# Kernel optimization log

Hardware: AMD Instinct MI355X
Metric: run time of the kernel (lower is better)

The kernel has to match this reference:

```python
import jax, jax.numpy as jnp
import numpy as np
from jax import lax

BZ, CAP, SEQ, INV = 32, 134, 144, 16
E_SP, E_FT = 1072, 64


def sage(x, e_src, e_dst, Wl, bl, Wr, n_nodes):
    # PyG SAGEConv (mean aggr): out = lin_l(mean_{j->i} x_j) + lin_r(x_i)
    # x: [B, N, F]; edges broadcast over batch
    msgs = x[:, e_src]                                   # [B, E, F] gather
    agg = jnp.zeros_like(x).at[:, e_dst].add(msgs)        # [B, N, F] scatter-add
    deg = jnp.zeros((n_nodes,), x.dtype).at[e_dst].add(1.0)
    mean = agg / jnp.clip(deg, 1.0)[None, :, None]
    return mean @ Wl + bl + x @ Wr


def setup_inputs() -> dict:
    key = jax.random.key(0)
    ks = jax.random.split(key, 16)
    s = lambda fan: 1.0 / np.sqrt(fan)
    inp = {
        'src': jax.random.normal(ks[0], (BZ, CAP, SEQ, INV), jnp.float32),
        'graph_edge_index': jax.random.randint(ks[1], (2, E_SP), 0, CAP, jnp.int32),
        'feature_edge_index': jax.random.randint(ks[2], (2, E_FT), 0, INV, jnp.int32),
        # spatial SAGEConv(in_var, in_var)
        'gcn_Wl': jax.random.uniform(ks[3], (INV, INV), jnp.float32, -s(INV), s(INV)),
        'gcn_bl': jnp.zeros((INV,), jnp.float32),
        'gcn_Wr': jax.random.uniform(ks[4], (INV, INV), jnp.float32, -s(INV), s(INV)),
        # feature SAGEConv(seq_len, seq_len)
        'fgcn_Wl': jax.random.uniform(ks[5], (SEQ, SEQ), jnp.float32, -s(SEQ), s(SEQ)),
        'fgcn_bl': jnp.zeros((SEQ,), jnp.float32),
        'fgcn_Wr': jax.random.uniform(ks[6], (SEQ, SEQ), jnp.float32, -s(SEQ), s(SEQ)),
        # Conv1d(in_var, in_var, k=3/5, no bias): OIW layout
        'conv1_w': jax.random.uniform(ks[7], (INV, INV, 3), jnp.float32, -s(INV * 3), s(INV * 3)),
        'conv2_w': jax.random.uniform(ks[8], (INV, INV, 5), jnp.float32, -s(INV * 5), s(INV * 5)),
        # Linear(3*in_var, in_var)
        'fc_w': jax.random.uniform(ks[9], (3 * INV, INV), jnp.float32, -s(3 * INV), s(3 * INV)),
        'fc_b': jnp.zeros((INV,), jnp.float32),
    }
    return inp


def reference(src, graph_edge_index, feature_edge_index, gcn_Wl, gcn_bl, gcn_Wr,
              fgcn_Wl, fgcn_bl, fgcn_Wr, conv1_w, conv2_w, fc_w, fc_b):
    bz, cap, seq, inv = src.shape
    # --- spatial GCN: nodes = turbines, features = in_var, batched over bz*seq
    x1 = src.transpose(0, 2, 1, 3).reshape(bz * seq, cap, inv)
    sp = sage(x1, graph_edge_index[0], graph_edge_index[1], gcn_Wl, gcn_bl, gcn_Wr, cap)
    spatial_fea = sp.reshape(bz, seq, cap, inv).transpose(0, 2, 1, 3)
    # --- feature GCN: nodes = variables, features = seq_len, batched over bz*cap
    x2 = src.transpose(0, 1, 3, 2).reshape(bz * cap, inv, seq)
    ft = sage(x2, feature_edge_index[0], feature_edge_index[1], fgcn_Wl, fgcn_bl, fgcn_Wr, inv)
    fea_fea = ft.reshape(bz, cap, inv, seq).transpose(0, 1, 3, 2)
    # --- temporal dual Conv1d over seq axis, channels = in_var
    x3 = src.reshape(bz * cap, seq, inv).transpose(0, 2, 1)  # [N, C, L]
    dn = ('NCH', 'OIH', 'NCH')
    c1 = lax.conv_general_dilated(x3, conv1_w, (1,), [(1, 1)], dimension_numbers=dn)
    c2 = lax.conv_general_dilated(x3, conv2_w, (1,), [(2, 2)], dimension_numbers=dn)
    temporal_fea = (c1 + c2).transpose(0, 2, 1).reshape(bz, cap, seq, inv)
    # --- concat + FC fusion + residual (dropout = identity at eval)
    com = jnp.concatenate([spatial_fea, fea_fea, temporal_fea], axis=-1)  # [..., 3*inv]
    out = com @ fc_w + fc_b
    return src + out
```

## Files before the change

kernel.cpp:

```cpp
#include <hip/hip_runtime.h>
#include <hip/hip_bf16.h>

#define BZn 32
#define CAPn 134
#define SEQn 144
#define INVn 16
#define ESP 1072
#define EFT 64


typedef __attribute__((ext_vector_type(8))) short bf16x8;
typedef __attribute__((ext_vector_type(4))) short short4v;
typedef __attribute__((ext_vector_type(4))) float f32x4;

#define MFMA(a, b, c) __builtin_amdgcn_mfma_f32_16x16x32_bf16(a, b, c, 0, 0, 0)

__device__ __forceinline__ unsigned short f2bf(float f) {
    union { float f; unsigned u; } v; v.f = f;
    unsigned r = v.u + 0x7fff + ((v.u >> 16) & 1);
    return (unsigned short)(r >> 16);
}
__device__ __forceinline__ unsigned pk2(float a, float b) {
    float2 v; v.x = a; v.y = b;
    union { __hip_bfloat162 h; unsigned u; } c;
    c.h = __float22bfloat162_rn(v);
    return c.u;
}
__device__ __forceinline__ short4v pack4(f32x4 v) {
    union { unsigned u[2]; short4v s; } r;
    r.u[0] = pk2(v[0], v[1]);
    r.u[1] = pk2(v[2], v[3]);
    return r.s;
}

__global__ __launch_bounds__(256) void prep_kernel(
    const int* __restrict__ ge, const int* __restrict__ fe,
    const float* __restrict__ Wl,  const float* __restrict__ Wr,
    const float* __restrict__ fWl, const float* __restrict__ fWr,
    const float* __restrict__ w1,  const float* __restrict__ w2,
    const float* __restrict__ fcw, const float* __restrict__ bl,
    const float* __restrict__ fcb,
    int* __restrict__ ws)
{
    int t = threadIdx.x;
    char* wsb = (char*)ws;
    unsigned short* uB     = (unsigned short*)(wsb + 5376);
    unsigned short* vB     = (unsigned short*)(wsb + 6400);
    unsigned short* spB2   = (unsigned short*)(wsb + 7424);
    float*          biasf  = (float*)(wsb + 8448);
    unsigned short* convA2 = (unsigned short*)(wsb + 8704);
    unsigned short* featB  = (unsigned short*)(wsb + 12800);

    if (blockIdx.x == 0) {
        int* g_rp  = ws;
        int* g_col = ws + 135;
        float* g_inv = (float*)(ws + 1207);
        __shared__ int cnt[CAPn], off[CAPn];
        for (int c0 = t; c0 < CAPn; c0 += 256) cnt[c0] = 0;
        __syncthreads();
        for (int e = t; e < ESP; e += 256) atomicAdd(&cnt[ge[ESP + e]], 1);
        __syncthreads();
        if (t == 0) {
            int run = 0;
            for (int c0 = 0; c0 < CAPn; c0++) {
                off[c0] = run; g_rp[c0] = run;
                g_inv[c0] = 1.0f / fmaxf((float)cnt[c0], 1.0f);
                run += cnt[c0];
            }
            g_rp[CAPn] = run;
        }
        __syncthreads();
        for (int c0 = t; c0 < CAPn; c0 += 256) cnt[c0] = 0;
        __syncthreads();
        for (int e = t; e < ESP; e += 256) {
            int d = ge[ESP + e];
            int p = off[d] + atomicAdd(&cnt[d], 1);
            g_col[p] = ge[e];
        }
    } else if (blockIdx.x == 1) {
        __shared__ float sw[1312];
        __shared__ int fm[256];
        __shared__ float finv[16];
        for (int u = t; u < 768; u += 256) sw[u] = fcw[u];
        if (t < 256) sw[768 + t]  = Wl[t];
        if (t < 256) sw[1024 + t] = Wr[t];
        if (t < 16)  sw[1280 + t] = bl[t];
        if (t < 16)  sw[1296 + t] = fcb[t];
        fm[t] = 0;
        __syncthreads();
        if (t < EFT) atomicAdd(&fm[fe[t] * 16 + fe[EFT + t]], 1);
        __syncthreads();
        if (t < 16) {
            int dg = 0;
            for (int j = 0; j < 16; j++) dg += fm[j * 16 + t];
            finv[t] = 1.0f / fmaxf((float)dg, 1.0f);
        }
        __syncthreads();
        for (int u = t; u < 512; u += 256) {
            int l = u >> 3, j = u & 7, k = (l >> 4) * 8 + j, ip = l & 15;
            float vu = 0.f, vv = 0.f, vs = 0.f;
            if (k < 16) {
                for (int i = 0; i < 16; i++)
                    vu += (float)fm[k * 16 + i] * finv[i] * sw[(16 + i) * 16 + ip];
                vv = sw[(16 + k) * 16 + ip];
                for (int i = 0; i < 16; i++) vs += sw[768 + k * 16 + i] * sw[i * 16 + ip];
            } else {
                for (int i = 0; i < 16; i++) vs += sw[1024 + (k - 16) * 16 + i] * sw[i * 16 + ip];
            }
            uB[u] = f2bf(vu); vB[u] = f2bf(vv); spB2[u] = f2bf(vs);
        }
        if (t < 16) {
            float b0 = sw[1296 + t], c0 = 0.f;
            for (int i = 0; i < 16; i++) {
                b0 += sw[1280 + i] * sw[i * 16 + t];
                c0 += sw[(16 + i) * 16 + t];
            }
            biasf[t] = b0; biasf[16 + t] = c0;
        }
    } else if (blockIdx.x == 2) {
        __shared__ float swt[2816];
        for (int u = t; u < 768;  u += 256) swt[u]        = fcw[u];
        for (int u = t; u < 768;  u += 256) swt[768 + u]  = w1[u];
        for (int u = t; u < 1280; u += 256) swt[1536 + u] = w2[u];
        __syncthreads();
        for (int u = t; u < 2048; u += 256) {
            int kk2 = u >> 9, l = (u >> 3) & 63, j = u & 7, q = l >> 4, o = l & 15;
            int kkp = kk2 * 2 + (q >> 1), i = (q & 1) * 8 + j;
            float v = 0.f;
            for (int o0 = 0; o0 < 16; o0++) {
                float w = (kkp < 3) ? swt[768 + (o0 * 16 + i) * 3 + kkp]
                                    : swt[1536 + (o0 * 16 + i) * 5 + (kkp - 3)];
                v += w * swt[(32 + o0) * 16 + o];
            }
            convA2[u] = f2bf(v);
        }
    } else {
        __shared__ float wtile[32][145];
        int kk = blockIdx.x - 3;
        for (int u = t; u < 32 * 144; u += 256) {
            int r = u / 144, s = u - r * 144;
            int k = kk * 32 + r;
            wtile[r][s] = (k < 144) ? fWl[k * 144 + s] : fWr[(k - 144) * 144 + s];
        }
        __syncthreads();
        for (int u = t; u < 4608; u += 256) {
            int n0 = u >> 9, rem = u & 511;
            int l = rem >> 3, j = rem & 7;
            featB[(kk * 9 + n0) * 512 + rem] =
                f2bf(wtile[(l >> 4) * 8 + j][n0 * 16 + (l & 15)]);
        }
    }
}

__global__ __launch_bounds__(256, 4) void fused_kernel(
    const float* __restrict__ src,
    const float* __restrict__ fbl,
    const int* __restrict__ ws,
    float* __restrict__ out)
{
    const int* g_rp  = ws;
    const int* g_col = ws + 135;
    const float* g_inv = (const float*)(ws + 1207);
    const char* wsb = (const char*)ws;
    const unsigned short* uB     = (const unsigned short*)(wsb + 5376);
    const unsigned short* vB     = (const unsigned short*)(wsb + 6400);
    const unsigned short* spB2   = (const unsigned short*)(wsb + 7424);
    const float*          biasf  = (const float*)(wsb + 8448);
    const unsigned short* convA2 = (const unsigned short*)(wsb + 8704);
    const unsigned short* featB  = (const unsigned short*)(wsb + 12800);

    __shared__ __align__(16) char smem[24704];
    unsigned short* xs = (unsigned short*)smem;
    unsigned short* mt = (unsigned short*)(smem + 7104);
    unsigned short* uv = (unsigned short*)(smem + 14016);
    float* accF   = (float*)smem;
    float* s_fbl  = (float*)(smem + 24000);
    float* s_bias = (float*)(smem + 24576);
    float* s_cs   = (float*)(smem + 24640);

    int t = threadIdx.x;
    int wave = t >> 6, lane = t & 63;
    int q = lane >> 4, ln = lane & 15;

    int ust_w = (wave == 0) ? 0 : (2 * wave + 1);
    int sst_w = 2 * wave;

    int xcd  = blockIdx.x & 7;
    int slot = blockIdx.x >> 3;
    int bl_  = slot / 134;
    int c    = slot - bl_ * 134;
    int b    = xcd * 4 + bl_;
    int bc   = b * CAPn + c;
    const float* srcb = src + (size_t)b * (CAPn * SEQn * INVn);
    const float* srcc = srcb + (size_t)c * (SEQn * INVn);

    const f32x4* s4 = (const f32x4*)srcc;
    f32x4 x0 = s4[t], x1 = s4[t + 256];
    f32x4 x2 = {0.f,0.f,0.f,0.f};
    if (t < 64) x2 = s4[t + 512];

    int rs = g_rp[c], re = g_rp[c + 1];
    float idg = g_inv[c];
    f32x4 m0a = {0.f,0.f,0.f,0.f}, m1a = {0.f,0.f,0.f,0.f}, m2a = {0.f,0.f,0.f,0.f};
    f32x4 m0b = {0.f,0.f,0.f,0.f}, m1b = {0.f,0.f,0.f,0.f}, m2b = {0.f,0.f,0.f,0.f};
    int e = rs;
    for (; e + 3 < re; e += 4) {
        int n0_ = g_col[e], n1_ = g_col[e + 1], n2_ = g_col[e + 2], n3_ = g_col[e + 3];
        const f32x4* p0 = (const f32x4*)(srcb + (size_t)n0_ * (SEQn * INVn));
        const f32x4* p1 = (const f32x4*)(srcb + (size_t)n1_ * (SEQn * INVn));
        const f32x4* p2 = (const f32x4*)(srcb + (size_t)n2_ * (SEQn * INVn));
        const f32x4* p3 = (const f32x4*)(srcb + (size_t)n3_ * (SEQn * INVn));
        f32x4 a0 = p0[t],       a1 = p1[t],       a2 = p2[t],       a3 = p3[t];
        f32x4 b0 = p0[t + 256], b1 = p1[t + 256], b2 = p2[t + 256], b3 = p3[t + 256];
        f32x4 c0 = {0.f,0.f,0.f,0.f}, c1 = c0, c2 = c0, c3 = c0;
        if (t < 64) { c0 = p0[t + 512]; c1 = p1[t + 512]; c2 = p2[t + 512]; c3 = p3[t + 512]; }
        m0a += a0; m0b += a1; m1a += b0; m1b += b1;
        m0a += a2; m0b += a3; m1a += b2; m1b += b3;
        if (t < 64) { m2a += c0; m2b += c1; m2a += c2; m2b += c3; }
    }
    for (; e + 1 < re; e += 2) {
        int na = g_col[e], nb = g_col[e + 1];
        const f32x4* pa = (const f32x4*)(srcb + (size_t)na * (SEQn * INVn));
        const f32x4* pb = (const f32x4*)(srcb + (size_t)nb * (SEQn * INVn));
        m0a += pa[t];       m0b += pb[t];
        m1a += pa[t + 256]; m1b += pb[t + 256];
        if (t < 64) { m2a += pa[t + 512]; m2b += pb[t + 512]; }
    }
    if (e < re) {
        int na = g_col[e];
        const f32x4* pa = (const f32x4*)(srcb + (size_t)na * (SEQn * INVn));
        m0a += pa[t]; m1a += pa[t + 256];
        if (t < 64) m2a += pa[t + 512];
    }

    bf16x8 caf0 = *(const bf16x8*)(convA2 + (0 * 64 + lane) * 8);
    bf16x8 caf1 = *(const bf16x8*)(convA2 + (1 * 64 + lane) * 8);
    bf16x8 caf2 = *(const bf16x8*)(convA2 + (2 * 64 + lane) * 8);
    bf16x8 caf3 = *(const bf16x8*)(convA2 + (3 * 64 + lane) * 8);
    bf16x8 sbf = *(const bf16x8*)(spB2 + lane * 8);
    bf16x8 ubf = *(const bf16x8*)(uB + lane * 8);
    bf16x8 vbf = *(const bf16x8*)(vB + lane * 8);

    int s0g = t >> 2, i0g = (t & 3) * 4;
    f32x4 m0 = (m0a + m0b) * idg, m1 = (m1a + m1b) * idg, m2 = (m2a + m2b) * idg;
    *(short4v*)&mt[s0g * 24 + i0g]         = pack4(m0);
    *(short4v*)&mt[(64 + s0g) * 24 + i0g]  = pack4(m1);
    if (t < 64) *(short4v*)&mt[(128 + s0g) * 24 + i0g] = pack4(m2);

    *(short4v*)&xs[(s0g + 2) * 24 + i0g]        = pack4(x0);
    *(short4v*)&xs[(64 + s0g + 2) * 24 + i0g]   = pack4(x1);
    if (t < 64) *(short4v*)&xs[(128 + s0g + 2) * 24 + i0g] = pack4(x2);
    if (t < 64) {
        int r = t >> 4, i = t & 15;
        int row = (r < 2) ? r : 144 + r;
        xs[row * 24 + i] = 0;
    }
    if (t < SEQn) s_fbl[t] = fbl[t];
    if (t < 16) { s_bias[t] = biasf[t]; s_cs[t] = biasf[16 + t]; }
    __syncthreads();

    #pragma unroll
    for (int tt = 0; tt < 3; tt++) {
        if ((wave == 0) || (tt < 2)) {
            int mtt = ust_w + tt;
            int sl = mtt * 16 + ln;
            bf16x8 a = {0,0,0,0,0,0,0,0};
            if (q < 2) a = *(const bf16x8*)&xs[(sl + 2) * 24 + q * 8];
            f32x4 au = {0.f,0.f,0.f,0.f}, av = {0.f,0.f,0.f,0.f};
            au = MFMA(a, ubf, au);
            av = MFMA(a, vbf, av);
            *(short4v*)&uv[ln * 312 + mtt * 16 + q * 4]       = pack4(au);
            *(short4v*)&uv[ln * 312 + 144 + mtt * 16 + q * 4] = pack4(av);
        }
    }
    f32x4 accS0 = {0.f,0.f,0.f,0.f}, accS1 = accS0, accS2 = accS0;
    {
        int sl = (sst_w + 0) * 16 + ln;
        const unsigned short* ap = (q < 2) ? &mt[sl * 24 + (q & 1) * 8]
                                           : &xs[(sl + 2) * 24 + (q & 1) * 8];
        accS0 = MFMA(*(const bf16x8*)ap, sbf, accS0);
    }
    {
        int sl = (sst_w + 1) * 16 + ln;
        const unsigned short* ap = (q < 2) ? &mt[sl * 24 + (q & 1) * 8]
                                           : &xs[(sl + 2) * 24 + (q & 1) * 8];
        accS1 = MFMA(*(const bf16x8*)ap, sbf, accS1);
    }
    if (wave == 3) {
        int sl = (sst_w + 2) * 16 + ln;
        const unsigned short* ap = (q < 2) ? &mt[sl * 24 + (q & 1) * 8]
                                           : &xs[(sl + 2) * 24 + (q & 1) * 8];
        accS2 = MFMA(*(const bf16x8*)ap, sbf, accS2);
    }
    __syncthreads();

#define B_TILE(N0, ACC) { \
    int n0_t = (N0); int sl_t = n0_t * 16 + ln; \
    bf16x8 bfrag[9]; \
    _Pragma("unroll") \
    for (int kk = 0; kk < 9; kk++) \
        bfrag[kk] = *(const bf16x8*)(featB + ((kk * 9 + n0_t) * 64 + lane) * 8); \
    bf16x8 cb[4]; \
    _Pragma("unroll") \
    for (int kk = 0; kk < 4; kk++) { \
        int kkp = kk * 2 + (q >> 1); \
        int off = (kkp < 3) ? (kkp - 1) : (kkp - 5); \
        cb[kk] = *(const bf16x8*)&xs[(sl_t + 2 + off) * 24 + (q & 1) * 8]; } \
    f32x4 acc_ = {0.f,0.f,0.f,0.f}; \
    acc_ = MFMA(caf0, cb[0], acc_); \
    acc_ = MFMA(caf1, cb[1], acc_); \
    acc_ = MFMA(caf2, cb[2], acc_); \
    acc_ = MFMA(caf3, cb[3], acc_); \
    _Pragma("unroll") \
    for (int kk = 0; kk < 9; kk++) { \
        bf16x8 a_ = *(const bf16x8*)&uv[ln * 312 + kk * 32 + q * 8]; \
        acc_ = MFMA(a_, bfrag[kk], acc_); } \
    ACC = acc_; }

    f32x4 accB0 = {0.f,0.f,0.f,0.f}, accB1 = accB0, accB2 = accB0;
    B_TILE(ust_w + 0, accB0)
    B_TILE(ust_w + 1, accB1)
    if (wave == 0) B_TILE(ust_w + 2, accB2)
#undef B_TILE
    __syncthreads();

    *(f32x4*)&accF[(((ust_w + 0) * 16 + ln) * 16) + q * 4] = accB0;
    *(f32x4*)&accF[(((ust_w + 1) * 16 + ln) * 16) + q * 4] = accB1;
    if (wave == 0)
        *(f32x4*)&accF[(((ust_w + 2) * 16 + ln) * 16) + q * 4] = accB2;
    __syncthreads();

    #pragma unroll
    for (int r = 0; r < 4; r++)
        accF[((sst_w + 0) * 16 + q * 4 + r) * 16 + ln] += accS0[r];
    #pragma unroll
    for (int r = 0; r < 4; r++)
        accF[((sst_w + 1) * 16 + q * 4 + r) * 16 + ln] += accS1[r];
    if (wave == 3) {
        #pragma unroll
        for (int r = 0; r < 4; r++)
            accF[((sst_w + 2) * 16 + q * 4 + r) * 16 + ln] += accS2[r];
    }
    __syncthreads();

    f32x4* out4 = (f32x4*)(out + (size_t)bc * (SEQn * INVn));
    int i0 = (t & 3) * 4;
    f32x4 bias4 = *(const f32x4*)&s_bias[i0];
    f32x4 cs4   = *(const f32x4*)&s_cs[i0];
    {
        f32x4 a = *(const f32x4*)&accF[4 * t];
        out4[t] = a + x0 + bias4 + s_fbl[t >> 2] * cs4;
    }
    {
        f32x4 a = *(const f32x4*)&accF[4 * (t + 256)];
        out4[t + 256] = a + x1 + bias4 + s_fbl[(t + 256) >> 2] * cs4;
    }
    if (t < 64) {
        f32x4 a = *(const f32x4*)&accF[4 * (t + 512)];
        out4[t + 512] = a + x2 + bias4 + s_fbl[(t + 512) >> 2] * cs4;
    }
}

extern "C" void kernel_launch(void* const* d_in, const int* in_sizes, int n_in,
                              void* d_out, int out_size, void* d_ws, size_t ws_size,
                              hipStream_t stream)
{
    const float* src = (const float*)d_in[0];
    const int* ge = (const int*)d_in[1];
    const int* fe = (const int*)d_in[2];
    const float* Wl  = (const float*)d_in[3];
    const float* blp = (const float*)d_in[4];
    const float* Wr  = (const float*)d_in[5];
    const float* fWl = (const float*)d_in[6];
    const float* fbl = (const float*)d_in[7];
    const float* fWr = (const float*)d_in[8];
    const float* w1  = (const float*)d_in[9];
    const float* w2  = (const float*)d_in[10];
    const float* fcw = (const float*)d_in[11];
    const float* fcb = (const float*)d_in[12];
    float* out = (float*)d_out;
    int* ws = (int*)d_ws;

    hipLaunchKernelGGL(prep_kernel, dim3(12), dim3(256), 0, stream,
                       ge, fe, Wl, Wr, fWl, fWr, w1, w2, fcw, blp, fcb, ws);
    hipLaunchKernelGGL(fused_kernel, dim3(BZn * CAPn), dim3(256), 0, stream,
                       src, fbl, ws, out);
}
```

Before: 150.8 us.

## Replace mean-tile LDS staging with cross-lane bpermute and pad accumulator rows

The neighbour-mean tile is no longer written to shared memory and read back for the spatial MFMA. Each wave now pulls its operands straight from registers with ds_bpermute, reassigning tiles so every wave handles the rows it already holds. This cuts LDS footprint, which may allow more resident blocks, and removes one store/load round trip. The fp32 accumulator buffer also gets a 20-float row stride instead of 16 to reduce bank conflicts in the transposed adds, at the cost of bpermute instructions and more index arithmetic.

After: 150.7 us. Within noise of the previous version (-0.0%).

```diff
diff --git a/kernel.cpp b/kernel.cpp
--- a/kernel.cpp
+++ b/kernel.cpp
@@ -169,21 +169,19 @@
     const unsigned short* convA2 = (const unsigned short*)(wsb + 8704);
     const unsigned short* featB  = (const unsigned short*)(wsb + 12800);
 
-    __shared__ __align__(16) char smem[24704];
+    __shared__ __align__(16) char smem[17792];
     unsigned short* xs = (unsigned short*)smem;
-    unsigned short* mt = (unsigned short*)(smem + 7104);
-    unsigned short* uv = (unsigned short*)(smem + 14016);
+    unsigned short* uv = (unsigned short*)(smem + 7104);
     float* accF   = (float*)smem;
-    float* s_fbl  = (float*)(smem + 24000);
-    float* s_bias = (float*)(smem + 24576);
-    float* s_cs   = (float*)(smem + 24640);
+    float* s_fbl  = (float*)(smem + 17088);
+    float* s_bias = (float*)(smem + 17664);
+    float* s_cs   = (float*)(smem + 17728);
 
     int t = threadIdx.x;
     int wave = t >> 6, lane = t & 63;
     int q = lane >> 4, ln = lane & 15;
 
     int ust_w = (wave == 0) ? 0 : (2 * wave + 1);
-    int sst_w = 2 * wave;
 
     int xcd  = blockIdx.x & 7;
     int slot = blockIdx.x >> 3;
@@ -241,12 +239,12 @@
     bf16x8 ubf = *(const bf16x8*)(uB + lane * 8);
     bf16x8 vbf = *(const bf16x8*)(vB + lane * 8);
 
+    f32x4 m0 = (m0a + m0b) * idg, m1 = (m1a + m1b) * idg, m2 = (m2a + m2b) * idg;
+    unsigned pA0 = pk2(m0[0], m0[1]), pB0 = pk2(m0[2], m0[3]);
+    unsigned pA1 = pk2(m1[0], m1[1]), pB1 = pk2(m1[2], m1[3]);
+    unsigned pA2 = pk2(m2[0], m2[1]), pB2 = pk2(m2[2], m2[3]);
+
     int s0g = t >> 2, i0g = (t & 3) * 4;
-    f32x4 m0 = (m0a + m0b) * idg, m1 = (m1a + m1b) * idg, m2 = (m2a + m2b) * idg;
-    *(short4v*)&mt[s0g * 24 + i0g]         = pack4(m0);
-    *(short4v*)&mt[(64 + s0g) * 24 + i0g]  = pack4(m1);
-    if (t < 64) *(short4v*)&mt[(128 + s0g) * 24 + i0g] = pack4(m2);
-
     *(short4v*)&xs[(s0g + 2) * 24 + i0g]        = pack4(x0);
     *(short4v*)&xs[(64 + s0g + 2) * 24 + i0g]   = pack4(x1);
     if (t < 64) *(short4v*)&xs[(128 + s0g + 2) * 24 + i0g] = pack4(x2);
@@ -273,25 +271,28 @@
             *(short4v*)&uv[ln * 312 + 144 + mtt * 16 + q * 4] = pack4(av);
         }
     }
+
+#define SP_TILE(T, PA, PB, ACC) { \
+    int base4 = (ln * 4 + 2 * q) * 4; \
+    int d0 = __builtin_amdgcn_ds_bpermute(base4,     (int)(PA)); \
+    int d1 = __builtin_amdgcn_ds_bpermute(base4,     (int)(PB)); \
+    int d2 = __builtin_amdgcn_ds_bpermute(base4 + 4, (int)(PA)); \
+    int d3 = __builtin_amdgcn_ds_bpermute(base4 + 4, (int)(PB)); \
+    bf16x8 a_; \
+    if (q < 2) { \
+        union { int i_[4]; bf16x8 v_; } u_; \
+        u_.i_[0] = d0; u_.i_[1] = d1; u_.i_[2] = d2; u_.i_[3] = d3; \
+        a_ = u_.v_; \
+    } else { \
+        a_ = *(const bf16x8*)&xs[((T) * 16 + ln + 2) * 24 + (q & 1) * 8]; \
+    } \
+    ACC = MFMA(a_, sbf, ACC); }
+
     f32x4 accS0 = {0.f,0.f,0.f,0.f}, accS1 = accS0, accS2 = accS0;
-    {
-        int sl = (sst_w + 0) * 16 + ln;
-        const unsigned short* ap = (q < 2) ? &mt[sl * 24 + (q & 1) * 8]
-                                           : &xs[(sl + 2) * 24 + (q & 1) * 8];
-        accS0 = MFMA(*(const bf16x8*)ap, sbf, accS0);
-    }
-    {
-        int sl = (sst_w + 1) * 16 + ln;
-        const unsigned short* ap = (q < 2) ? &mt[sl * 24 + (q & 1) * 8]
-                                           : &xs[(sl + 2) * 24 + (q & 1) * 8];
-        accS1 = MFMA(*(const bf16x8*)ap, sbf, accS1);
-    }
-    if (wave == 3) {
-        int sl = (sst_w + 2) * 16 + ln;
-        const unsigned short* ap = (q < 2) ? &mt[sl * 24 + (q & 1) * 8]
-                                           : &xs[(sl + 2) * 24 + (q & 1) * 8];
-        accS2 = MFMA(*(const bf16x8*)ap, sbf, accS2);
-    }
+    SP_TILE(wave,     pA0, pB0, accS0)
+    SP_TILE(wave + 4, pA1, pB1, accS1)
+    if (wave == 0) SP_TILE(8, pA2, pB2, accS2)
+#undef SP_TILE
     __syncthreads();
 
 #define B_TILE(N0, ACC) { \
@@ -324,22 +325,22 @@
 #undef B_TILE
     __syncthreads();
 
-    *(f32x4*)&accF[(((ust_w + 0) * 16 + ln) * 16) + q * 4] = accB0;
-    *(f32x4*)&accF[(((ust_w + 1) * 16 + ln) * 16) + q * 4] = accB1;
+    *(f32x4*)&accF[((ust_w + 0) * 16 + ln) * 20 + q * 4] = accB0;
+    *(f32x4*)&accF[((ust_w + 1) * 16 + ln) * 20 + q * 4] = accB1;
     if (wave == 0)
-        *(f32x4*)&accF[(((ust_w + 2) * 16 + ln) * 16) + q * 4] = accB2;
+        *(f32x4*)&accF[((ust_w + 2) * 16 + ln) * 20 + q * 4] = accB2;
     __syncthreads();
 
     #pragma unroll
     for (int r = 0; r < 4; r++)
-        accF[((sst_w + 0) * 16 + q * 4 + r) * 16 + ln] += accS0[r];
+        accF[(wave * 16 + q * 4 + r) * 20 + ln] += accS0[r];
     #pragma unroll
     for (int r = 0; r < 4; r++)
-        accF[((sst_w + 1) * 16 + q * 4 + r) * 16 + ln] += accS1[r];
-    if (wave == 3) {
+        accF[((wave + 4) * 16 + q * 4 + r) * 20 + ln] += accS1[r];
+    if (wave == 0) {
         #pragma unroll
         for (int r = 0; r < 4; r++)
-            accF[((sst_w + 2) * 16 + q * 4 + r) * 16 + ln] += accS2[r];
+            accF[(128 + q * 4 + r) * 20 + ln] += accS2[r];
     }
     __syncthreads();
 
@@ -348,16 +349,18 @@
     f32x4 bias4 = *(const f32x4*)&s_bias[i0];
     f32x4 cs4   = *(const f32x4*)&s_cs[i0];
     {
-        f32x4 a = *(const f32x4*)&accF[4 * t];
+        f32x4 a = *(const f32x4*)&accF[(t >> 2) * 20 + i0];
         out4[t] = a + x0 + bias4 + s_fbl[t >> 2] * cs4;
     }
     {
-        f32x4 a = *(const f32x4*)&accF[4 * (t + 256)];
-        out4[t + 256] = a + x1 + bias4 + s_fbl[(t + 256) >> 2] * cs4;
+        int t1 = t + 256;
+        f32x4 a = *(const f32x4*)&accF[(t1 >> 2) * 20 + i0];
+        out4[t1] = a + x1 + bias4 + s_fbl[t1 >> 2] * cs4;
     }
     if (t < 64) {
-        f32x4 a = *(const f32x4*)&accF[4 * (t + 512)];
-        out4[t + 512] = a + x2 + bias4 + s_fbl[(t + 512) >> 2] * cs4;
+        int t2 = t + 512;
+        f32x4 a = *(const f32x4*)&accF[(t2 >> 2) * 20 + i0];
+        out4[t2] = a + x2 + bias4 + s_fbl[t2 >> 2] * cs4;
     }
 }
 
```
